# Performance work log

Measured on AMD Instinct MI355X. Metric: run time of the kernel, lower is better.

The kernel has to match this reference:

```python
import jax, jax.numpy as jnp
import numpy as np

N = 200_000   # nodes
E = 6_400_000 # edges (avg degree 32)
G = 1024      # graphs in the batch
H = 8         # hidden dim


def setup_inputs() -> dict:
    key = jax.random.key(0)
    ks = jax.random.split(key, 13)
    x = jax.random.normal(ks[0], (N, 1), dtype=jnp.float32)
    edge_index = jax.random.randint(ks[1], (2, E), 0, N, dtype=jnp.int32)
    batch = jnp.sort(jax.random.randint(ks[2], (N,), 0, G, dtype=jnp.int32))
    s = 0.3
    params = dict(
        W1a=s * jax.random.normal(ks[3], (1, H), jnp.float32),
        b1a=jnp.zeros((H,), jnp.float32),
        W1b=s * jax.random.normal(ks[4], (H, H), jnp.float32),
        b1b=jnp.zeros((H,), jnp.float32),
        W2a=s * jax.random.normal(ks[5], (H, H), jnp.float32),
        b2a=jnp.zeros((H,), jnp.float32),
        W2b=s * jax.random.normal(ks[6], (H, H), jnp.float32),
        b2b=jnp.zeros((H,), jnp.float32),
        Wfc=s * jax.random.normal(ks[7], (H, 1), jnp.float32),
        bfc=jnp.zeros((1,), jnp.float32),
    )
    return dict(x=x, edge_index=edge_index, batch=batch, **params)


def _gin_layer(h, src, dst, Wa, ba, Wb, bb):
    # GINConv with eps=0: mlp(x_i + sum_{j->i} x_j); messages aggregated at dst=edge_index[1]
    agg = jax.ops.segment_sum(h[src], dst, num_segments=N)  # [N, d]
    z = h + agg
    z = jax.nn.relu(z @ Wa + ba)
    return z @ Wb + bb


def reference(x, edge_index, batch, W1a, b1a, W1b, b1b, W2a, b2a, W2b, b2b, Wfc, bfc):
    src, dst = edge_index[0], edge_index[1]
    h = _gin_layer(x, src, dst, W1a, b1a, W1b, b1b)   # [N, 8]
    h = jax.nn.elu(h)
    h = _gin_layer(h, src, dst, W2a, b2a, W2b, b2b)   # [N, 8]
    # global mean pool over graphs
    sums = jax.ops.segment_sum(h, batch, num_segments=G)                  # [G, 8]
    counts = jax.ops.segment_sum(jnp.ones((N,), h.dtype), batch, num_segments=G)
    pooled = sums / jnp.maximum(counts, 1.0)[:, None]
    out = jax.nn.sigmoid(pooled @ Wfc + bfc)          # [G, 1]
    return out.reshape(-1)
```

## Files before the change

kernel.cpp:

```cpp
#include <hip/hip_runtime.h>
#include <hip/hip_fp8.h>
#include <math.h>

#define H 8
#define NBLKA 256
#define BTH 1024
#define BSH 8
#define BCAP 9216
#define TS 1024
#define CAP 14336
#define SCAP 25600
#define POOLG 128
#define NPB2 128

__device__ __forceinline__ unsigned f2fp8(float f) {
    __hip_fp8_e4m3 q(f);
    return (unsigned)q.__x;
}
__device__ __forceinline__ float fp8f(unsigned v) {
    __hip_fp8_e4m3 q;
    q.__x = (__hip_fp8_storage_t)v;
    return (float)q;
}

__global__ __launch_bounds__(BTH) void scatterK(const int* __restrict__ ei, int E, int NB,
                                                int chunk, int* __restrict__ cursor,
                                                unsigned* __restrict__ packed) {
    __shared__ unsigned ss[SCAP];
    __shared__ int cnt[1024], sc[1024], base[1024], cur[1024];
    int t = threadIdx.x, blk = blockIdx.x;
    cnt[t] = 0;
    __syncthreads();
    int s = blk * chunk, e = min(E, s + chunk);
    for (int i = s + t; i < e; i += BTH)
        atomicAdd(&cnt[__builtin_nontemporal_load(ei + E + i) >> BSH], 1);
    __syncthreads();
    int c = cnt[t];
    sc[t] = c;
    __syncthreads();
    for (int off = 1; off < 1024; off <<= 1) {
        int v = (t >= off) ? sc[t - off] : 0;
        __syncthreads();
        sc[t] += v;
        __syncthreads();
    }
    cur[t] = sc[t] - c;
    base[t] = (t < NB && c > 0) ? atomicAdd(&cursor[t], c) : 0;
    __syncthreads();
    for (int i = s + t; i < e; i += BTH) {
        int src = __builtin_nontemporal_load(ei + i);
        int dst = __builtin_nontemporal_load(ei + E + i);
        int pos = atomicAdd(&cur[dst >> BSH], 1);
        ss[pos] = ((unsigned)src << 8) | (unsigned)(dst & 255);
    }
    __syncthreads();
    int wave = t >> 6, lane = t & 63;
    for (int j = wave; j < NB; j += (BTH >> 6)) {
        int n = cnt[j];
        int ls = sc[j] - n;
        int bs = base[j];
        int m = min(n, BCAP - bs);
        int gs = j * BCAP + bs;
        for (int k = lane; k < m; k += 64)
            packed[gs + k] = ss[ls + k];
    }
}

__global__ void sortL1K(unsigned* __restrict__ packed, const int* __restrict__ bucketCnt,
                        const float* __restrict__ x, int N,
                        const float* __restrict__ W1a, const float* __restrict__ b1a,
                        const float* __restrict__ W1b, const float* __restrict__ b1b,
                        int* __restrict__ nodeStart, uint2* __restrict__ h1) {
    __shared__ unsigned ss[CAP];
    __shared__ int cnt[256], sb[256], cur[256];
    __shared__ float sW1a[H], sb1a[H], sW1b[H * H], sb1b[H];
    int t = threadIdx.x, b = blockIdx.x;
    if (t < 256) cnt[t] = 0;
    else if (t < 256 + H) { int j = t - 256; sW1a[j] = W1a[j]; sb1a[j] = b1a[j]; sb1b[j] = b1b[j]; }
    else if (t < 256 + H + H * H) { int j = t - 256 - H; sW1b[j] = W1b[j]; }
    __syncthreads();
    int s = b * BCAP;
    int n_e = min(bucketCnt[b], BCAP);
    for (int i = t; i < n_e; i += TS)
        atomicAdd(&cnt[__builtin_nontemporal_load(packed + s + i) & 255u], 1);
    __syncthreads();
    if (t < 256) sb[t] = cnt[t];
    __syncthreads();
    for (int off = 1; off < 256; off <<= 1) {
        int add = (t < 256 && t >= off) ? sb[t - off] : 0;
        __syncthreads();
        if (t < 256) sb[t] += add;
        __syncthreads();
    }
    if (t < 256) {
        int excl = sb[t] - cnt[t];
        cur[t] = excl;
        nodeStart[(b << BSH) + t] = s + excl;
    }
    __syncthreads();
    for (int i = t; i < n_e; i += TS) {
        unsigned p = __builtin_nontemporal_load(packed + s + i);
        int pos = atomicAdd(&cur[p & 255u], 1);
        ss[pos] = p >> 8;
    }
    __syncthreads();
    for (int i = t; i < n_e; i += TS) packed[s + i] = ss[i];
    int node = t >> 2, q4 = t & 3;
    int gn = (b << BSH) + node;
    int lo = sb[node] - cnt[node], hi = sb[node];
    float sum = 0.f;
    for (int k = lo + q4; k < hi; k += 4) sum += x[ss[k]];
    sum += __shfl_xor(sum, 1, 64);
    sum += __shfl_xor(sum, 2, 64);
    if (q4 == 0 && gn < N) {
        float z = x[gn] + sum;
        float tv[H];
#pragma unroll
        for (int k = 0; k < H; k++) tv[k] = fmaxf(fmaf(z, sW1a[k], sb1a[k]), 0.f);
        float hv[H];
#pragma unroll
        for (int j = 0; j < H; j++) {
            float a = sb1b[j];
#pragma unroll
            for (int k = 0; k < H; k++) a += tv[k] * sW1b[k * H + j];
            hv[j] = a > 0.f ? a : (expf(a) - 1.f);
        }
        uint2 o;
        o.x = f2fp8(hv[0]) | (f2fp8(hv[1]) << 8) | (f2fp8(hv[2]) << 16) | (f2fp8(hv[3]) << 24);
        o.y = f2fp8(hv[4]) | (f2fp8(hv[5]) << 8) | (f2fp8(hv[6]) << 16) | (f2fp8(hv[7]) << 24);
        h1[gn] = o;
    }
}

__global__ __launch_bounds__(1024) void layer2K(
        const unsigned* __restrict__ srcSorted, const int* __restrict__ nodeStart,
        const int* __restrict__ bucketCnt, const uint2* __restrict__ h1, int N,
        const float* __restrict__ W2a, const float* __restrict__ b2a,
        const float* __restrict__ W2b, const float* __restrict__ b2b,
        const int* __restrict__ batch, float* __restrict__ sumsCnt) {
    __shared__ float pool[POOLG * 9];
    __shared__ float sW2a[H * H], sb2a[H], sW2b[H * H], sb2b[H];
    int t = threadIdx.x, b = blockIdx.x;
    if (t < H) { sb2a[t] = b2a[t]; sb2b[t] = b2b[t]; }
    else if (t >= 64 && t < 64 + H * H) sW2a[t - 64] = W2a[t - 64];
    else if (t >= 192 && t < 192 + H * H) sW2b[t - 192] = W2b[t - 192];
    __syncthreads();
    int node = t >> 3, lane8 = t & 7;
    int gn = b * NPB2 + node;
    int segS = nodeStart[gn];
    int segE = ((gn & 255) == 255)
                 ? (gn >> 8) * BCAP + min(bucketCnt[gn >> 8], BCAP)
                 : nodeStart[gn + 1];
    float a[H] = {0.f, 0.f, 0.f, 0.f, 0.f, 0.f, 0.f, 0.f};
    for (int k = segS + lane8; k < segE; k += 8) {
        uint2 v = h1[__builtin_nontemporal_load(srcSorted + k)];
        a[0] += fp8f(v.x & 255u);         a[1] += fp8f((v.x >> 8) & 255u);
        a[2] += fp8f((v.x >> 16) & 255u); a[3] += fp8f(v.x >> 24);
        a[4] += fp8f(v.y & 255u);         a[5] += fp8f((v.y >> 8) & 255u);
        a[6] += fp8f((v.y >> 16) & 255u); a[7] += fp8f(v.y >> 24);
    }
#pragma unroll
    for (int j = 0; j < H; j++) {
        a[j] += __shfl_xor(a[j], 1, 64);
        a[j] += __shfl_xor(a[j], 2, 64);
        a[j] += __shfl_xor(a[j], 4, 64);
    }
    bool valid = (lane8 == 0) && (gn < N);
    float h2[H];
    int g = 0;
    if (valid) {
        uint2 v = h1[gn];
        float z[H] = {fp8f(v.x & 255u) + a[0],         fp8f((v.x >> 8) & 255u) + a[1],
                      fp8f((v.x >> 16) & 255u) + a[2], fp8f(v.x >> 24) + a[3],
                      fp8f(v.y & 255u) + a[4],         fp8f((v.y >> 8) & 255u) + a[5],
                      fp8f((v.y >> 16) & 255u) + a[6], fp8f(v.y >> 24) + a[7]};
        float tv[H];
#pragma unroll
        for (int k = 0; k < H; k++) {
            float acc = sb2a[k];
#pragma unroll
            for (int j = 0; j < H; j++) acc += z[j] * sW2a[j * H + k];
            tv[k] = fmaxf(acc, 0.f);
        }
#pragma unroll
        for (int j = 0; j < H; j++) {
            float acc = sb2b[j];
#pragma unroll
            for (int k = 0; k < H; k++) acc += tv[k] * sW2b[k * H + j];
            h2[j] = acc;
        }
        g = batch[gn];
    }
    int gfirst = batch[min(b * NPB2, N - 1)];
    int glast  = batch[min(b * NPB2 + NPB2 - 1, N - 1)];
    int span = glast - gfirst + 1;
    if (span <= POOLG) {
        int span9 = span * 9;
        for (int j = t; j < span9; j += 1024) pool[j] = 0.f;
        __syncthreads();
        if (valid) {
            float* p = &pool[(g - gfirst) * 9];
#pragma unroll
            for (int j = 0; j < H; j++) atomicAdd(p + j, h2[j]);
            atomicAdd(p + 8, 1.f);
        }
        __syncthreads();
        for (int j = t; j < span9; j += 1024)
            atomicAdd(&sumsCnt[(size_t)gfirst * 9 + j], pool[j]);
    } else if (valid) {
        float* p = &sumsCnt[(size_t)g * 9];
#pragma unroll
        for (int j = 0; j < H; j++) atomicAdd(p + j, h2[j]);
        atomicAdd(p + 8, 1.f);
    }
}

__global__ void finalK(const float* __restrict__ sumsCnt, const float* __restrict__ Wfc,
                       const float* __restrict__ bfc, float* __restrict__ out, int G) {
    int g = blockIdx.x * blockDim.x + threadIdx.x;
    if (g >= G) return;
    const float* s = &sumsCnt[(size_t)g * 9];
    float c = fmaxf(s[8], 1.f);
    float dot = 0.f;
#pragma unroll
    for (int j = 0; j < H; j++) dot += s[j] * Wfc[j];
    float a = dot / c + bfc[0];
    out[g] = 1.f / (1.f + expf(-a));
}

__global__ void edge_agg1(const int* __restrict__ ei, const float* __restrict__ x,
                          float* __restrict__ agg1, int E) {
    int e = blockIdx.x * blockDim.x + threadIdx.x;
    if (e >= E) return;
    atomicAdd(&agg1[ei[E + e]], x[ei[e]]);
}
__global__ void node1F(const float* __restrict__ x, const float* __restrict__ agg1,
                       const float* __restrict__ W1a, const float* __restrict__ b1a,
                       const float* __restrict__ W1b, const float* __restrict__ b1b,
                       float* __restrict__ h1, int N) {
    int n = blockIdx.x * blockDim.x + threadIdx.x;
    if (n >= N) return;
    float z = x[n] + agg1[n];
    float tv[H];
#pragma unroll
    for (int k = 0; k < H; k++) tv[k] = fmaxf(z * W1a[k] + b1a[k], 0.f);
#pragma unroll
    for (int j = 0; j < H; j++) {
        float acc = b1b[j];
#pragma unroll
        for (int k = 0; k < H; k++) acc += tv[k] * W1b[k * H + j];
        h1[(size_t)n * H + j] = acc > 0.f ? acc : (expf(acc) - 1.f);
    }
}
__global__ void edge_agg2(const int* __restrict__ ei, const float* __restrict__ h1,
                          float* __restrict__ agg2, int E) {
    long long i = (long long)blockIdx.x * blockDim.x + threadIdx.x;
    if (i >= (long long)E * H) return;
    int e = (int)(i >> 3), k = (int)(i & 7);
    atomicAdd(&agg2[(size_t)ei[E + e] * H + k], h1[(size_t)ei[e] * H + k]);
}
__global__ void node2F(const float* __restrict__ h1, const float* __restrict__ agg2,
                       const float* __restrict__ W2a, const float* __restrict__ b2a,
                       const float* __restrict__ W2b, const float* __restrict__ b2b,
                       const int* __restrict__ batch,
                       float* __restrict__ sums, float* __restrict__ counts, int N) {
    int n = blockIdx.x * blockDim.x + threadIdx.x;
    if (n >= N) return;
    float z[H], tv[H];
#pragma unroll
    for (int j = 0; j < H; j++) z[j] = h1[(size_t)n * H + j] + agg2[(size_t)n * H + j];
#pragma unroll
    for (int k = 0; k < H; k++) {
        float a = b2a[k];
#pragma unroll
        for (int j = 0; j < H; j++) a += z[j] * W2a[j * H + k];
        tv[k] = fmaxf(a, 0.f);
    }
    int g = batch[n];
#pragma unroll
    for (int j = 0; j < H; j++) {
        float a = b2b[j];
#pragma unroll
        for (int k = 0; k < H; k++) a += tv[k] * W2b[k * H + j];
        atomicAdd(&sums[(size_t)g * H + j], a);
    }
    atomicAdd(&counts[g], 1.f);
}
__global__ void finalF(const float* __restrict__ sums, const float* __restrict__ counts,
                       const float* __restrict__ Wfc, const float* __restrict__ bfc,
                       float* __restrict__ out, int G) {
    int g = blockIdx.x * blockDim.x + threadIdx.x;
    if (g >= G) return;
    float c = fmaxf(counts[g], 1.f);
    float acc = bfc[0];
#pragma unroll
    for (int j = 0; j < H; j++) acc += (sums[(size_t)g * H + j] / c) * Wfc[j];
    out[g] = 1.f / (1.f + expf(-acc));
}

extern "C" void kernel_launch(void* const* d_in, const int* in_sizes, int n_in,
                              void* d_out, int out_size, void* d_ws, size_t ws_size,
                              hipStream_t stream) {
    const float* x    = (const float*)d_in[0];
    const int*   ei   = (const int*)d_in[1];
    const int*   batch= (const int*)d_in[2];
    const float* W1a  = (const float*)d_in[3];
    const float* b1a  = (const float*)d_in[4];
    const float* W1b  = (const float*)d_in[5];
    const float* b1b  = (const float*)d_in[6];
    const float* W2a  = (const float*)d_in[7];
    const float* b2a  = (const float*)d_in[8];
    const float* W2b  = (const float*)d_in[9];
    const float* b2b  = (const float*)d_in[10];
    const float* Wfc  = (const float*)d_in[11];
    const float* bfc  = (const float*)d_in[12];

    const int N = in_sizes[0];
    const int E = in_sizes[1] / 2;
    const int G = out_size;
    const int NB = (N + 255) >> BSH;
    const int chunk = (E + NBLKA - 1) / NBLKA;
    const int B = 256;

    auto rnd4 = [](size_t v) { return (v + 3) & ~(size_t)3; };
    size_t o_cur  = 0;
    size_t o_sc   = 1024;
    size_t zelems = o_sc + (size_t)9 * G;
    size_t o_ns   = rnd4(zelems);
    size_t o_h1   = rnd4(o_ns + ((size_t)NB << BSH) + 1);
    size_t o_pk   = rnd4(o_h1 + ((size_t)NB << BSH) * 2);
    size_t total  = o_pk + (size_t)NB * BCAP;

    bool srcFits = (N <= (1 << 18));
    bool chunkFits = (chunk <= SCAP);
    bool capOK = ((size_t)E / NB) * 10 <= (size_t)BCAP * 9;
    if (NB <= 1024 && srcFits && chunkFits && capOK && ws_size >= total * 4) {
        int*      wsi = (int*)d_ws;
        float*    wsf = (float*)d_ws;
        unsigned* wsu = (unsigned*)d_ws;
        int*      cursor    = wsi + o_cur;
        float*    sumsCnt   = wsf + o_sc;
        int*      nodeStart = wsi + o_ns;
        uint2*    h1        = (uint2*)(wsu + o_h1);
        unsigned* packed    = wsu + o_pk;

        hipMemsetAsync(d_ws, 0, zelems * 4, stream);
        scatterK<<<NBLKA, BTH, 0, stream>>>(ei, E, NB, chunk, cursor, packed);
        sortL1K<<<NB, TS, 0, stream>>>(packed, cursor, x, N, W1a, b1a, W1b, b1b,
                                       nodeStart, h1);
        layer2K<<<(N + NPB2 - 1) / NPB2, 1024, 0, stream>>>(packed, nodeStart, cursor, h1,
                                                            N, W2a, b2a, W2b, b2b,
                                                            batch, sumsCnt);
        finalK<<<(G + B - 1) / B, B, 0, stream>>>(sumsCnt, Wfc, bfc, (float*)d_out, G);
    } else {
        float* ws     = (float*)d_ws;
        float* agg1   = ws;
        float* agg2   = agg1 + (size_t)N;
        float* sums   = agg2 + (size_t)8 * N;
        float* counts = sums + (size_t)8 * G;
        float* h1     = counts + (size_t)G;
        hipMemsetAsync(ws, 0, ((size_t)9 * N + (size_t)9 * G) * sizeof(float), stream);
        edge_agg1<<<(E + B - 1) / B, B, 0, stream>>>(ei, x, agg1, E);
        node1F<<<(N + B - 1) / B, B, 0, stream>>>(x, agg1, W1a, b1a, W1b, b1b, h1, N);
        long long tot = (long long)E * H;
        edge_agg2<<<(int)((tot + B - 1) / B), B, 0, stream>>>(ei, h1, agg2, E);
        node2F<<<(N + B - 1) / B, B, 0, stream>>>(h1, agg2, W2a, b2a, W2b, b2b, batch,
                                                  sums, counts, N);
        finalF<<<(G + B - 1) / B, B, 0, stream>>>(sums, counts, Wfc, bfc, (float*)d_out, G);
    }
}
```

Measured before the change: 278.9 us.

## Stage whole dst bucket's sorted edges in LDS for layer-2 aggregation

layer2K now runs one block per 256-node bucket instead of per 128 nodes. Each block first stages the bucket's sorted source indices and node offsets into shared memory with coalesced loads, then gathers using 4 lanes per node instead of 8. This replaces scattered per-node index reads from global memory with one contiguous load, and halves the shuffle reduction. In exchange it uses about 37KB of LDS per block, which can lower occupancy, and lanes idle more on high-degree nodes.

Result: faster. 266.1 us (-4.6%).

```diff
diff --git a/kernel.cpp b/kernel.cpp
--- a/kernel.cpp
+++ b/kernel.cpp
@@ -11,7 +11,6 @@
 #define CAP 14336
 #define SCAP 25600
 #define POOLG 128
-#define NPB2 128
 
 __device__ __forceinline__ unsigned f2fp8(float f) {
     __hip_fp8_e4m3 q(f);
@@ -133,27 +132,34 @@
 }
 
 __global__ __launch_bounds__(1024) void layer2K(
-        const unsigned* __restrict__ srcSorted, const int* __restrict__ nodeStart,
+        const unsigned* __restrict__ packed, const int* __restrict__ nodeStart,
         const int* __restrict__ bucketCnt, const uint2* __restrict__ h1, int N,
         const float* __restrict__ W2a, const float* __restrict__ b2a,
         const float* __restrict__ W2b, const float* __restrict__ b2b,
         const int* __restrict__ batch, float* __restrict__ sumsCnt) {
+    __shared__ unsigned ss[BCAP];
+    __shared__ int sNS[257];
     __shared__ float pool[POOLG * 9];
     __shared__ float sW2a[H * H], sb2a[H], sW2b[H * H], sb2b[H];
     int t = threadIdx.x, b = blockIdx.x;
+    int s = b * BCAP;
+    int n_e = min(bucketCnt[b], BCAP);
+    for (int i = t; i < n_e; i += 1024)
+        ss[i] = __builtin_nontemporal_load(packed + s + i);
+    if (t < 256) sNS[t] = nodeStart[(b << BSH) + t] - s;
+    if (t == 256) sNS[256] = 0;
     if (t < H) { sb2a[t] = b2a[t]; sb2b[t] = b2b[t]; }
     else if (t >= 64 && t < 64 + H * H) sW2a[t - 64] = W2a[t - 64];
     else if (t >= 192 && t < 192 + H * H) sW2b[t - 192] = W2b[t - 192];
     __syncthreads();
-    int node = t >> 3, lane8 = t & 7;
-    int gn = b * NPB2 + node;
-    int segS = nodeStart[gn];
-    int segE = ((gn & 255) == 255)
-                 ? (gn >> 8) * BCAP + min(bucketCnt[gn >> 8], BCAP)
-                 : nodeStart[gn + 1];
+    if (t == 0) sNS[256] = n_e;
+    __syncthreads();
+    int node = t >> 2, q4 = t & 3;
+    int gn = (b << BSH) + node;
+    int lo = sNS[node], hi = sNS[node + 1];
     float a[H] = {0.f, 0.f, 0.f, 0.f, 0.f, 0.f, 0.f, 0.f};
-    for (int k = segS + lane8; k < segE; k += 8) {
-        uint2 v = h1[__builtin_nontemporal_load(srcSorted + k)];
+    for (int k = lo + q4; k < hi; k += 4) {
+        uint2 v = h1[ss[k]];
         a[0] += fp8f(v.x & 255u);         a[1] += fp8f((v.x >> 8) & 255u);
         a[2] += fp8f((v.x >> 16) & 255u); a[3] += fp8f(v.x >> 24);
         a[4] += fp8f(v.y & 255u);         a[5] += fp8f((v.y >> 8) & 255u);
@@ -163,9 +169,8 @@
     for (int j = 0; j < H; j++) {
         a[j] += __shfl_xor(a[j], 1, 64);
         a[j] += __shfl_xor(a[j], 2, 64);
-        a[j] += __shfl_xor(a[j], 4, 64);
-    }
-    bool valid = (lane8 == 0) && (gn < N);
+    }
+    bool valid = (q4 == 0) && (gn < N);
     float h2[H];
     int g = 0;
     if (valid) {
@@ -191,8 +196,8 @@
         }
         g = batch[gn];
     }
-    int gfirst = batch[min(b * NPB2, N - 1)];
-    int glast  = batch[min(b * NPB2 + NPB2 - 1, N - 1)];
+    int gfirst = batch[min(b << BSH, N - 1)];
+    int glast  = batch[min((b << BSH) + 255, N - 1)];
     int span = glast - gfirst + 1;
     if (span <= POOLG) {
         int span9 = span * 9;
@@ -348,9 +353,8 @@
         scatterK<<<NBLKA, BTH, 0, stream>>>(ei, E, NB, chunk, cursor, packed);
         sortL1K<<<NB, TS, 0, stream>>>(packed, cursor, x, N, W1a, b1a, W1b, b1b,
                                        nodeStart, h1);
-        layer2K<<<(N + NPB2 - 1) / NPB2, 1024, 0, stream>>>(packed, nodeStart, cursor, h1,
-                                                            N, W2a, b2a, W2b, b2b,
-                                                            batch, sumsCnt);
+        layer2K<<<NB, 1024, 0, stream>>>(packed, nodeStart, cursor, h1, N,
+                                         W2a, b2a, W2b, b2b, batch, sumsCnt);
         finalK<<<(G + B - 1) / B, B, 0, stream>>>(sumsCnt, Wfc, bfc, (float*)d_out, G);
     } else {
         float* ws     = (float*)d_ws;
```
